# Performance work log

Hardware: AMD Instinct MI355X
Metric: run time of the kernel (lower is better)

The kernel has to match this reference:

```python
import jax, jax.numpy as jnp
import numpy as np

N_EMBED = 1024
HEAD_SIZE = 64


def setup_inputs() -> dict:
    key = jax.random.key(0)
    kx, kk, kq, kv = jax.random.split(key, 4)
    B, T = 8, 2048
    x = jax.random.normal(kx, (B, T, N_EMBED), dtype=jnp.float32)
    # nn.Linear weights, stored as (in, out) so projection is x @ W
    s = 1.0 / np.sqrt(N_EMBED)
    Wk = jax.random.uniform(kk, (N_EMBED, HEAD_SIZE), jnp.float32, -s, s)
    Wq = jax.random.uniform(kq, (N_EMBED, HEAD_SIZE), jnp.float32, -s, s)
    Wv = jax.random.uniform(kv, (N_EMBED, HEAD_SIZE), jnp.float32, -s, s)
    return {"x": x, "Wk": Wk, "Wq": Wq, "Wv": Wv}


def reference(x, Wk, Wq, Wv):
    # x: [B, T, C] with C = n_embed
    C = x.shape[-1]
    k = x @ Wk  # [B, T, H]
    q = x @ Wq  # [B, T, H]
    v = x @ Wv  # [B, T, H]
    # NOTE: original scales by n_embed**-0.5, not head_size**-0.5
    wei = jnp.einsum("bth,bsh->bts", q, k) * (C ** -0.5)  # [B, T, T]
    wei = jax.nn.softmax(wei, axis=-1)
    # dropout = 0.0 (eval mode) -> identity
    out = jnp.einsum("bts,bsh->bth", wei, v)  # [B, T, H]
    return out
```

## Files before the change

### kernel.cpp

```cpp
#include <hip/hip_runtime.h>
#include <stdint.h>


#define B_ 8
#define T_ 2048
#define C_ 1024
#define H_ 64

typedef float f32x4 __attribute__((ext_vector_type(4)));
typedef short s16x8 __attribute__((ext_vector_type(8)));

__device__ __forceinline__ unsigned int rhu16(float f) {
    return (__float_as_uint(f) + 0x8000u) >> 16;
}
__device__ __forceinline__ unsigned int pkbf(float lo, float hi) {
    unsigned int a = __float_as_uint(lo) + 0x8000u;
    unsigned int b = __float_as_uint(hi) + 0x8000u;
    return __builtin_amdgcn_perm(b, a, 0x07060302u);
}
__device__ __forceinline__ void ld_lds16(const void* g, void* l) {
    __builtin_amdgcn_global_load_lds(
        (const __attribute__((address_space(1))) unsigned int*)g,
        (__attribute__((address_space(3))) unsigned int*)l, 16, 0, 0);
}

__global__ __launch_bounds__(256) void wconv(const float* __restrict__ Wk,
        const float* __restrict__ Wq, const float* __restrict__ Wv,
        unsigned short* __restrict__ Wt) {
    __shared__ float ls[64 * 65];
    const int bx = blockIdx.x, t = threadIdx.x;
    const int mat = bx >> 4, c0 = (bx & 15) << 6;
    const float* W = (mat == 0) ? Wk : ((mat == 1) ? Wq : Wv);
    const float sc = (mat == 1) ? 0.03125f : 1.0f;
    #pragma unroll
    for (int k = 0; k < 4; k++) {
        int i = t + (k << 8);
        int cr = i >> 4, hq = (i & 15) << 2;
        float4 v = *reinterpret_cast<const float4*>(&W[(size_t)(c0 + cr) * H_ + hq]);
        ls[cr * 65 + hq + 0] = v.x; ls[cr * 65 + hq + 1] = v.y;
        ls[cr * 65 + hq + 2] = v.z; ls[cr * 65 + hq + 3] = v.w;
    }
    __syncthreads();
    #pragma unroll
    for (int k = 0; k < 4; k++) {
        int i = t + (k << 8);
        int h = i >> 4, cq = (i & 15) << 2;
        float a = ls[(cq + 0) * 65 + h] * sc, b = ls[(cq + 1) * 65 + h] * sc;
        float c = ls[(cq + 2) * 65 + h] * sc, d = ls[(cq + 3) * 65 + h] * sc;
        uint2 o; o.x = pkbf(a, b); o.y = pkbf(c, d);
        *reinterpret_cast<uint2*>(&Wt[(size_t)(mat * 64 + h) * C_ + c0 + cq]) = o;
    }
}

__global__ __launch_bounds__(512) __attribute__((amdgpu_waves_per_eu(4, 4)))
void qkv(const float* __restrict__ x,
        const unsigned short* __restrict__ Wt,
        unsigned short* __restrict__ kb, unsigned short* __restrict__ qb,
        unsigned short* __restrict__ vtb) {
    __shared__ __align__(16) char smem[65536];
    char* xb = smem;
    char* wb = smem + 16384;

    const int t = threadIdx.x, lane = t & 63, w = t >> 6;
    const int l15 = lane & 15, quad = lane >> 4;
    const int bx = blockIdx.x;
    const int bb = bx >> 6;
    const int mt = bx & 63;
    const int m0 = bb * T_ + mt * 32;
    const int wr = w >> 2;
    const int colb = (w & 3) * 48;

    size_t xg; int xl;
    {
        int rg = w >> 2, j = w & 3;
        xg = (size_t)(m0 + rg * 16 + l15) * C_ + j * 16 + quad * 4;
        xl = w * 1024 + lane * 16;
    }
    size_t wg[3]; int wl[3];
    #pragma unroll
    for (int n = 0; n < 3; n++) {
        int g = w * 3 + n;
        wg[n] = (size_t)(g * 8 + (lane & 7)) * C_ + (lane >> 3) * 8;
        wl[n] = g * 1024 + lane * 16;
    }

    ld_lds16(x + xg, xb + xl);
    #pragma unroll
    for (int n = 0; n < 3; n++) ld_lds16(Wt + wg[n], wb + wl[n]);

    f32x4 acc[3];
    #pragma unroll
    for (int ct = 0; ct < 3; ct++)
        #pragma unroll
        for (int j = 0; j < 4; j++) acc[ct][j] = 0.0f;

    #pragma unroll
    for (int i = 0; i < 16; i++) {
        const int cb = i & 1;

        asm volatile("s_waitcnt vmcnt(0)" ::: "memory");
        __builtin_amdgcn_sched_barrier(0);
        __builtin_amdgcn_s_barrier();
        __builtin_amdgcn_sched_barrier(0);

        if (i < 15) {
            const int c1 = (i + 1) * 64;
            char* xn = xb + (cb ^ 1) * 8192;
            char* wn = wb + (cb ^ 1) * 24576;
            ld_lds16(x + xg + c1, xn + xl);
            #pragma unroll
            for (int n = 0; n < 3; n++) ld_lds16(Wt + wg[n] + c1, wn + wl[n]);
        }
        __builtin_amdgcn_sched_barrier(0);

        const float* xc = (const float*)(xb + cb * 8192);
        const unsigned short* wcp = (const unsigned short*)(wb + cb * 24576);

        float4 xr[2][2];
        #pragma unroll
        for (int ks = 0; ks < 2; ks++)
            #pragma unroll
            for (int h = 0; h < 2; h++) {
                int c = ks * 32 + quad * 8 + h * 4;
                int j = c >> 4, u = (c & 15) >> 2;
                xr[ks][h] = *reinterpret_cast<const float4*>(
                    xc + (wr * 4 + j) * 256 + u * 64 + l15 * 4);
            }
        s16x8 wfr[3][2];
        #pragma unroll
        for (int ct = 0; ct < 3; ct++)
            #pragma unroll
            for (int ks = 0; ks < 2; ks++) {
                int col = colb + ct * 16 + l15;
                wfr[ct][ks] = *reinterpret_cast<const s16x8*>(
                    wcp + (col >> 3) * 512 + ((4 * ks + quad) * 8 + (col & 7)) * 8);
            }

        s16x8 af[2];
        #pragma unroll
        for (int ks = 0; ks < 2; ks++) {
            const float4 a = xr[ks][0], b = xr[ks][1];
            uint4 pk;
            pk.x = pkbf(a.x, a.y); pk.y = pkbf(a.z, a.w);
            pk.z = pkbf(b.x, b.y); pk.w = pkbf(b.z, b.w);
            af[ks] = *reinterpret_cast<s16x8*>(&pk);
        }
        #pragma unroll
        for (int ks = 0; ks < 2; ks++)
            #pragma unroll
            for (int ct = 0; ct < 3; ct++)
                acc[ct] = __builtin_amdgcn_mfma_f32_16x16x32_bf16(
                    af[ks], wfr[ct][ks], acc[ct], 0, 0, 0);
    }

    #pragma unroll
    for (int ct = 0; ct < 3; ct++) {
        int cbv = colb + ct * 16;
        int sel = cbv >> 6;
        int h = (cbv & 63) + l15;
        int row0 = m0 + wr * 16 + quad * 4;
        if (sel < 2) {
            unsigned short* dst = sel ? qb : kb;
            #pragma unroll
            for (int r = 0; r < 4; r++)
                dst[(size_t)(row0 + r) * H_ + h] = (unsigned short)rhu16(acc[ct][r]);
        } else {
            int tt = row0 - bb * T_;
            uint2 pk;
            pk.x = pkbf(acc[ct][0], acc[ct][1]);
            pk.y = pkbf(acc[ct][2], acc[ct][3]);
            *reinterpret_cast<uint2*>(&vtb[((size_t)bb * H_ + h) * T_ + tt]) = pk;
        }
    }
}

__global__ __launch_bounds__(512) __attribute__((amdgpu_waves_per_eu(2, 2)))
void attn(
        const unsigned short* __restrict__ qb,
        const unsigned short* __restrict__ kb,
        const unsigned short* __restrict__ vtb,
        float* __restrict__ out) {
    __shared__ __align__(16) char smem[137216];

    const int t = threadIdx.x, lane = t & 63, w = t >> 6;
    const int l15 = lane & 15, quad = lane >> 4;
    const int bb = blockIdx.x & 7;
    const int q0 = (blockIdx.x >> 3) << 6;
    const size_t kbase = (size_t)bb * T_ * H_;
    unsigned short* Pw = (unsigned short*)(smem + w * 9216);

    s16x8 qf[4][2];
    #pragma unroll
    for (int rt = 0; rt < 4; rt++)
        #pragma unroll
        for (int ks = 0; ks < 2; ks++)
            qf[rt][ks] = *reinterpret_cast<const s16x8*>(
                &qb[kbase + (size_t)(q0 + rt * 16 + l15) * H_ + ks * 32 + quad * 8]);

    const int sw = w << 8;
    const unsigned short* kq = kb + kbase + (size_t)(sw + l15) * H_ + quad * 8;
    const unsigned short* vq[4];
    #pragma unroll
    for (int ht = 0; ht < 4; ht++)
        vq[ht] = vtb + ((size_t)bb * H_ + ht * 16 + l15) * T_ + sw + quad * 8;

    f32x4 oacc[4][4];
    #pragma unroll
    for (int rt = 0; rt < 4; rt++)
        #pragma unroll
        for (int ht = 0; ht < 4; ht++)
            #pragma unroll
            for (int j = 0; j < 4; j++) oacc[rt][ht][j] = 0.0f;
    float l_run[4] = {0.0f, 0.0f, 0.0f, 0.0f};
    const f32x4 z4 = {0.0f, 0.0f, 0.0f, 0.0f};

    for (int it = 0; it < 4; it++) {
        s16x8 kf[4][2], vf[2][4];
        #pragma unroll
        for (int st = 0; st < 4; st++)
            #pragma unroll
            for (int ks = 0; ks < 2; ks++)
                kf[st][ks] = *reinterpret_cast<const s16x8*>(
                    kq + (size_t)(it * 64 + st * 16) * H_ + ks * 32);
        #pragma unroll
        for (int ks2 = 0; ks2 < 2; ks2++)
            #pragma unroll
            for (int ht = 0; ht < 4; ht++)
                vf[ks2][ht] = *reinterpret_cast<const s16x8*>(
                    vq[ht] + it * 64 + ks2 * 32);

        #pragma unroll
        for (int rt = 0; rt < 4; rt++) {
            f32x4 sacc[4];
            #pragma unroll
            for (int st = 0; st < 4; st++) {
                f32x4 s0v = __builtin_amdgcn_mfma_f32_16x16x32_bf16(
                    kf[st][0], qf[rt][0], z4, 0, 0, 0);
                sacc[st] = __builtin_amdgcn_mfma_f32_16x16x32_bf16(
                    kf[st][1], qf[rt][1], s0v, 0, 0, 0);
            }
            float ls = 0.0f;
            #pragma unroll
            for (int st = 0; st < 4; st++) {
                float p0 = __expf(sacc[st][0]);
                float p1 = __expf(sacc[st][1]);
                float p2 = __expf(sacc[st][2]);
                float p3 = __expf(sacc[st][3]);
                ls += (p0 + p1) + (p2 + p3);
                uint2 pk; pk.x = pkbf(p0, p1); pk.y = pkbf(p2, p3);
                *reinterpret_cast<uint2*>(
                    &Pw[(rt * 16 + l15) * 72 + st * 16 + quad * 4]) = pk;
            }
            l_run[rt] += ls;
        }

        #pragma unroll
        for (int rt = 0; rt < 4; rt++)
            #pragma unroll
            for (int ks2 = 0; ks2 < 2; ks2++) {
                s16x8 pf = *reinterpret_cast<const s16x8*>(
                    &Pw[(rt * 16 + l15) * 72 + ks2 * 32 + quad * 8]);
                #pragma unroll
                for (int ht = 0; ht < 4; ht++)
                    oacc[rt][ht] = __builtin_amdgcn_mfma_f32_16x16x32_bf16(
                        pf, vf[ks2][ht], oacc[rt][ht], 0, 0, 0);
            }
    }

    #pragma unroll
    for (int rt = 0; rt < 4; rt++) {
        l_run[rt] += __shfl_xor(l_run[rt], 16);
        l_run[rt] += __shfl_xor(l_run[rt], 32);
    }

    __syncthreads();
    float* Osf = (float*)smem;
    float* Ls  = (float*)smem + 8 * 64 * 66;
    #pragma unroll
    for (int rt = 0; rt < 4; rt++) {
        if (quad == 0) Ls[w * 64 + rt * 16 + l15] = l_run[rt];
        #pragma unroll
        for (int ht = 0; ht < 4; ht++)
            #pragma unroll
            for (int r = 0; r < 4; r++)
                Osf[(w * 64 + rt * 16 + quad * 4 + r) * 66 + ht * 16 + l15]
                    = oacc[rt][ht][r];
    }
    __syncthreads();
    #pragma unroll
    for (int rr = 0; rr < 8; rr++) {
        int row = w * 8 + rr;
        float lt = 0.0f, o = 0.0f;
        #pragma unroll
        for (int wv = 0; wv < 8; wv++) {
            lt += Ls[wv * 64 + row];
            o  += Osf[(wv * 64 + row) * 66 + lane];
        }
        out[kbase + (size_t)(q0 + row) * H_ + lane] = o * (1.0f / lt);
    }
}

extern "C" void kernel_launch(void* const* d_in, const int* in_sizes, int n_in,
                              void* d_out, int out_size, void* d_ws, size_t ws_size,
                              hipStream_t stream) {
    const float* x  = (const float*)d_in[0];
    const float* Wk = (const float*)d_in[1];
    const float* Wq = (const float*)d_in[2];
    const float* Wv = (const float*)d_in[3];

    unsigned short* kb  = (unsigned short*)d_ws;
    unsigned short* qbf = kb  + (size_t)B_ * T_ * H_;
    unsigned short* vtb = qbf + (size_t)B_ * T_ * H_;
    unsigned short* Wt  = (unsigned short*)d_out;

    wconv<<<48,  256, 0, stream>>>(Wk, Wq, Wv, Wt);
    qkv  <<<512, 512, 0, stream>>>(x, Wt, kb, qbf, vtb);
    attn <<<256, 512, 0, stream>>>(qbf, kb, vtb, (float*)d_out);
}
```

Before: 140.8 us.

## Store Q/K/V in MFMA-fragment-native tiled layout for contiguous per-lane loads

After: 136.7 us. -2.9%, faster.

```diff
diff --git a/kernel.cpp b/kernel.cpp
--- a/kernel.cpp
+++ b/kernel.cpp
@@ -157,19 +157,23 @@
     for (int ct = 0; ct < 3; ct++) {
         int cbv = colb + ct * 16;
         int sel = cbv >> 6;
-        int h = (cbv & 63) + l15;
-        int row0 = m0 + wr * 16 + quad * 4;
+        int hb = cbv & 63;
+        int h = hb + l15;
         if (sel < 2) {
             unsigned short* dst = sel ? qb : kb;
+            size_t base = ((size_t)(bb * 128 + mt * 2 + wr) * 8 + (h >> 3)) * 128
+                        + (quad * 4) * 8 + (h & 7);
             #pragma unroll
             for (int r = 0; r < 4; r++)
-                dst[(size_t)(row0 + r) * H_ + h] = (unsigned short)rhu16(acc[ct][r]);
+                dst[base + r * 8] = (unsigned short)rhu16(acc[ct][r]);
         } else {
-            int tt = row0 - bb * T_;
+            int thi = mt * 4 + wr * 2 + (quad >> 1);
+            size_t base = ((size_t)(bb * 4 + (h >> 4)) * 256 + thi) * 128
+                        + (h & 15) * 8 + (quad & 1) * 4;
             uint2 pk;
             pk.x = pkbf(acc[ct][0], acc[ct][1]);
             pk.y = pkbf(acc[ct][2], acc[ct][3]);
-            *reinterpret_cast<uint2*>(&vtb[((size_t)bb * H_ + h) * T_ + tt]) = pk;
+            *reinterpret_cast<uint2*>(&vtb[base]) = pk;
         }
     }
 }
@@ -185,24 +189,21 @@
     const int t = threadIdx.x, lane = t & 63, w = t >> 6;
     const int l15 = lane & 15, quad = lane >> 4;
     const int bb = blockIdx.x & 7;
-    const int q0 = (blockIdx.x >> 3) << 6;
+    const int qt = blockIdx.x >> 3;
+    const int q0 = qt << 6;
     const size_t kbase = (size_t)bb * T_ * H_;
     unsigned short* Pw = (unsigned short*)(smem + w * 9216);
 
+    const unsigned short* Qb = qb  + ((size_t)(bb * 128 + qt * 4) * 1024) + lane * 8;
+    const unsigned short* Kb = kb  + ((size_t)(bb * 128 + w * 16) * 1024) + lane * 8;
+    const unsigned short* Vb = vtb + ((size_t)(bb * 4) * 256 + w * 32) * 128 + lane * 8;
+
     s16x8 qf[4][2];
     #pragma unroll
     for (int rt = 0; rt < 4; rt++)
         #pragma unroll
         for (int ks = 0; ks < 2; ks++)
-            qf[rt][ks] = *reinterpret_cast<const s16x8*>(
-                &qb[kbase + (size_t)(q0 + rt * 16 + l15) * H_ + ks * 32 + quad * 8]);
-
-    const int sw = w << 8;
-    const unsigned short* kq = kb + kbase + (size_t)(sw + l15) * H_ + quad * 8;
-    const unsigned short* vq[4];
-    #pragma unroll
-    for (int ht = 0; ht < 4; ht++)
-        vq[ht] = vtb + ((size_t)bb * H_ + ht * 16 + l15) * T_ + sw + quad * 8;
+            qf[rt][ks] = *reinterpret_cast<const s16x8*>(Qb + rt * 1024 + ks * 512);
 
     f32x4 oacc[4][4];
     #pragma unroll
@@ -221,13 +222,13 @@
             #pragma unroll
             for (int ks = 0; ks < 2; ks++)
                 kf[st][ks] = *reinterpret_cast<const s16x8*>(
-                    kq + (size_t)(it * 64 + st * 16) * H_ + ks * 32);
+                    Kb + (it * 4 + st) * 1024 + ks * 512);
         #pragma unroll
         for (int ks2 = 0; ks2 < 2; ks2++)
             #pragma unroll
             for (int ht = 0; ht < 4; ht++)
                 vf[ks2][ht] = *reinterpret_cast<const s16x8*>(
-                    vq[ht] + it * 64 + ks2 * 32);
+                    Vb + ht * 32768 + it * 1024 + ks2 * 512);
 
         #pragma unroll
         for (int rt = 0; rt < 4; rt++) {
```
